# Kernel tuning notes

Measured on AMD Instinct MI355X. Metric: run time of the kernel, lower is better.

The kernel has to match this reference:

```python
import jax, jax.numpy as jnp
import numpy as np
import math

B, T, WIDTH, NUM_HEADS, WINDOW = 2, 2048, 1024, 16, 1024
HEAD_DIM = WIDTH // NUM_HEADS
_MIN_LOGITS_VALUE = -1e30


def setup_inputs() -> dict:
    key = jax.random.key(0)
    k1, k2, k3, k4, k5 = jax.random.split(key, 5)
    std = math.sqrt(1.0 / WIDTH)
    x = jax.random.normal(k1, (B, T, WIDTH), dtype=jnp.float32)
    segment_pos = jnp.tile(jnp.arange(T, dtype=jnp.int32)[None, :], (B, 1))
    Wq = jax.random.normal(k2, (WIDTH, WIDTH), dtype=jnp.float32) * std
    Wk = jax.random.normal(k3, (HEAD_DIM, WIDTH), dtype=jnp.float32) * std
    Wv = jax.random.normal(k4, (HEAD_DIM, WIDTH), dtype=jnp.float32) * std
    Wf = jax.random.normal(k5, (WIDTH, WIDTH), dtype=jnp.float32) * std
    bf = jnp.zeros((WIDTH,), dtype=jnp.float32)
    return {"x": x, "segment_pos": segment_pos, "Wq": Wq, "Wk": Wk, "Wv": Wv, "Wf": Wf, "bf": bf}


def reference(x, segment_pos, Wq, Wk, Wv, Wf, bf):
    b, t, _ = x.shape
    # projections (torch Linear: y = x @ W.T)
    q = (x @ Wq.T).reshape(b, t, NUM_HEADS, HEAD_DIM)  # b t n h
    k = x @ Wk.T  # b s h  (single shared KV head, MQA)
    v = x @ Wv.T  # b s h
    scale = 1.0 / math.sqrt(HEAD_DIM)
    logits = jnp.einsum('btnh,bsh->bnts', q, k) * scale
    pos = jnp.arange(t)
    q_pos = pos[:, None]
    k_pos = pos[None, :]
    mask = (q_pos >= k_pos) & (q_pos <= k_pos + WINDOW)  # [t, t]
    masked = jnp.where(mask[None, None, :, :], logits, _MIN_LOGITS_VALUE)
    probs = jax.nn.softmax(masked.astype(jnp.float32), axis=-1).astype(logits.dtype)
    out = jnp.einsum('bnts,bsh->btnh', probs, v).reshape(b, t, WIDTH)
    return out @ Wf.T + bf
```

## Files before the change

### kernel.cpp

```cpp
#include <hip/hip_runtime.h>
#include <cstdint>
#include <cstddef>

#define BB      2
#define TT      2048
#define WID     1024
#define NH      16
#define HD      64
#define WIN     1024
#define MROWS   (BB*TT)
#define NQKV    1152
#define QSCL    0.18033688011112042f

typedef __attribute__((ext_vector_type(8))) short  short8;
typedef __attribute__((ext_vector_type(4))) float  floatx4;

__device__ __forceinline__ unsigned short f2bf(float f) {
  union { float f; unsigned int u; } v; v.f = f;
  unsigned int u = v.u;
  unsigned int r = (u + 0x7fffu + ((u >> 16) & 1u)) >> 16;
  return (unsigned short)r;
}

__device__ __forceinline__ float fast_exp2(float x) {
#if __has_builtin(__builtin_amdgcn_exp2f)
  return __builtin_amdgcn_exp2f(x);
#else
  return exp2f(x);
#endif
}

__device__ __forceinline__ unsigned int pk_bf16_trunc(float lo, float hi) {
  union { float f; unsigned int u; } a, b; a.f = lo; b.f = hi;
#if __has_builtin(__builtin_amdgcn_perm)
  return __builtin_amdgcn_perm(b.u, a.u, 0x07060302u);
#else
  return (b.u & 0xffff0000u) | (a.u >> 16);
#endif
}

__device__ __forceinline__ void gld_lds16(const void* g, void* l) {
  __builtin_amdgcn_global_load_lds(
      (const __attribute__((address_space(1))) unsigned int*)g,
      (__attribute__((address_space(3))) unsigned int*)l, 16, 0, 0);
}

__global__ __launch_bounds__(256) void convert_kernel(
    const float* __restrict__ x,  const float* __restrict__ wq,
    const float* __restrict__ wk, const float* __restrict__ wv,
    const float* __restrict__ wf,
    unsigned short* __restrict__ xb, unsigned short* __restrict__ wb,
    unsigned short* __restrict__ wfb)
{
  const int NX4 = (MROWS * WID) / 4;
  const int NQ4 = (WID * WID) / 4;
  const int NK4 = (HD * WID) / 4;
  const int NW4 = NQ4 + 2 * NK4;
  const int NF4 = (WID * WID) / 4;
  const int TOT = NX4 + NW4 + NF4;
  for (int i = blockIdx.x * blockDim.x + threadIdx.x; i < TOT;
       i += gridDim.x * blockDim.x) {
    float4 v4;
    unsigned short* dptr;
    if (i < NX4) {
      v4 = ((const float4*)x)[i];
      dptr = xb + (size_t)i * 4;
    } else if (i < NX4 + NW4) {
      int k = i - NX4;
      dptr = wb + (size_t)k * 4;
      if (k < NQ4)            v4 = ((const float4*)wq)[k];
      else if (k < NQ4 + NK4) v4 = ((const float4*)wk)[k - NQ4];
      else                    v4 = ((const float4*)wv)[k - NQ4 - NK4];
    } else {
      int k = i - NX4 - NW4;
      v4 = ((const float4*)wf)[k];
      dptr = wfb + (size_t)k * 4;
    }
    ushort4 o4 = make_ushort4(f2bf(v4.x), f2bf(v4.y), f2bf(v4.z), f2bf(v4.w));
    *(ushort4*)dptr = o4;
  }
}

__global__ __launch_bounds__(256) void gemm128(
    const unsigned short* __restrict__ A, const unsigned short* __restrict__ Bm,
    int M, int N, int K, int mode,
    float* __restrict__ C, const float* __restrict__ bias,
    unsigned short* __restrict__ qb, unsigned short* __restrict__ kb,
    unsigned short* __restrict__ vtb)
{
  __shared__ __align__(16) unsigned short As[2][128 * 32];
  __shared__ __align__(16) unsigned short Bs[2][128 * 32];

  const int tid  = threadIdx.x;
  const int m0   = blockIdx.x * 128;
  const int n0   = blockIdx.y * 128;
  const int w    = tid >> 6;
  const int lane = tid & 63;
  const int wr   = w >> 1;
  const int wc   = w & 1;
  const int quad = lane >> 4;
  const int l16  = lane & 15;

  const int r0 = tid >> 2;
  const int c0 = (tid + r0) & 3;
  const unsigned short* gA0 = A  + (size_t)(m0 + r0) * K + c0 * 8;
  const unsigned short* gA1 = A  + (size_t)(m0 + r0 + 64) * K + c0 * 8;
  const unsigned short* gB0 = Bm + (size_t)(n0 + r0) * K + c0 * 8;
  const unsigned short* gB1 = Bm + (size_t)(n0 + r0 + 64) * K + c0 * 8;
  char* ldsA = (char*)As + (tid & 192) * 16;
  char* ldsB = (char*)Bs + (tid & 192) * 16;

  const int jsw = ((quad - l16) & 3) * 8;

  floatx4 acc[4][4];
#pragma unroll
  for (int it = 0; it < 4; ++it)
#pragma unroll
    for (int jt = 0; jt < 4; ++jt)
      acc[it][jt] = (floatx4){0.f, 0.f, 0.f, 0.f};

  const int K32 = K >> 5;
  gld_lds16(gA0, ldsA);
  gld_lds16(gA1, ldsA + 4096);
  gld_lds16(gB0, ldsB);
  gld_lds16(gB1, ldsB + 4096);
  __syncthreads();

  for (int kt = 0; kt < K32; ++kt) {
    const int cur = kt & 1;
    if (kt + 1 < K32) {
      const int nxt = cur ^ 1;
      const int off = (kt + 1) * 32;
      gld_lds16(gA0 + off, ldsA + nxt * 8192);
      gld_lds16(gA1 + off, ldsA + nxt * 8192 + 4096);
      gld_lds16(gB0 + off, ldsB + nxt * 8192);
      gld_lds16(gB1 + off, ldsB + nxt * 8192 + 4096);
    }
    const unsigned short* as = As[cur];
    const unsigned short* bs = Bs[cur];
    short8 af[4], bfr[4];
#pragma unroll
    for (int it = 0; it < 4; ++it)
      af[it] = *(const short8*)(as + (wr * 64 + it * 16 + l16) * 32 + jsw);
#pragma unroll
    for (int jt = 0; jt < 4; ++jt)
      bfr[jt] = *(const short8*)(bs + (wc * 64 + jt * 16 + l16) * 32 + jsw);

#pragma unroll
    for (int it = 0; it < 4; ++it)
#pragma unroll
      for (int jt = 0; jt < 4; ++jt)
        acc[it][jt] = __builtin_amdgcn_mfma_f32_16x16x32_bf16(
            af[it], bfr[jt], acc[it][jt], 0, 0, 0);
    __syncthreads();
  }

  if (mode == 0) {
#pragma unroll
    for (int it = 0; it < 4; ++it) {
      const int gr = m0 + wr * 64 + it * 16 + quad * 4;
#pragma unroll
      for (int jt = 0; jt < 4; ++jt) {
        const int gc = n0 + wc * 64 + jt * 16 + l16;
        const float badd = bias[gc];
#pragma unroll
        for (int r = 0; r < 4; ++r)
          C[(size_t)(gr + r) * N + gc] = acc[it][jt][r] + badd;
      }
    }
  } else {
#pragma unroll
    for (int it = 0; it < 4; ++it) {
      const int gr = m0 + wr * 64 + it * 16 + quad * 4;
#pragma unroll
      for (int jt = 0; jt < 4; ++jt) {
        const int gc = n0 + wc * 64 + jt * 16 + l16;
        if (gc < WID) {
#pragma unroll
          for (int r = 0; r < 4; ++r)
            qb[(size_t)(gr + r) * WID + gc] = f2bf(acc[it][jt][r] * QSCL);
        } else if (gc < WID + HD) {
#pragma unroll
          for (int r = 0; r < 4; ++r)
            kb[(size_t)(gr + r) * HD + (gc - WID)] = f2bf(acc[it][jt][r]);
        } else {
          ushort4 o4 = make_ushort4(f2bf(acc[it][jt][0]), f2bf(acc[it][jt][1]),
                                    f2bf(acc[it][jt][2]), f2bf(acc[it][jt][3]));
          *(ushort4*)(vtb + (size_t)(gc - WID - HD) * MROWS + gr) = o4;
        }
      }
    }
  }
}

__global__ __launch_bounds__(512) void attn_mfma(
    const unsigned short* __restrict__ qb, const unsigned short* __restrict__ kb,
    const unsigned short* __restrict__ vtb, unsigned short* __restrict__ attnb)
{
  __shared__ __align__(16) unsigned short smem[20480];

  const int tid  = threadIdx.x;
  const int w    = tid >> 6;
  const int g    = w >> 2;
  const int wh   = w & 3;
  const int lane = tid & 63;
  const int l16  = lane & 15;
  const int quad = lane >> 4;
  const int t0   = blockIdx.x * 32;
  const int h    = blockIdx.y * 4 + wh;
  const int b    = blockIdx.z;

  unsigned short* Ksb = smem;
  unsigned short* VTb = smem + 5120;
  unsigned short* Psb = smem + 10240 + w * 1280;

  short8 qf[2][2];
#pragma unroll
  for (int nt = 0; nt < 2; ++nt) {
    const unsigned short* qp =
        qb + (size_t)(b * TT + t0 + nt * 16 + l16) * WID + h * HD + quad * 8;
    qf[nt][0] = *(const short8*)qp;
    qf[nt][1] = *(const short8*)(qp + 32);
  }

  floatx4 Oacc[4][2];
#pragma unroll
  for (int mh = 0; mh < 4; ++mh)
#pragma unroll
    for (int nt = 0; nt < 2; ++nt)
      Oacc[mh][nt] = (floatx4){0.f, 0.f, 0.f, 0.f};
  float lq[2] = {0.f, 0.f};

  int s_begin = t0 - WIN; if (s_begin < 0) s_begin = 0;
  const int T = ((t0 + 32) - s_begin) >> 5;
  const int I = (T + 1) >> 1;

  const int kkey  = tid >> 3;
  const int khseg = (tid & 7) * 8;
  const int ksel  = kkey >> 5, krow = kkey & 31;
  const int vhd   = tid >> 3;
  const int vkk   = (tid & 7) * 8;
  const int vsel  = vkk >> 5,  vcol = vkk & 31;

  const unsigned short* kbase = kb  + (size_t)(b * TT) * HD;
  const unsigned short* vbase = vtb + (size_t)vhd * MROWS + b * TT;

  int s0p = s_begin;
  int ck = s0p + kkey; if (ck > TT - 1) ck = TT - 1;
  int cv = s0p + vkk;  if (cv > TT - 8) cv = TT - 8;
  short8 kreg = *(const short8*)(kbase + (size_t)ck * HD + khseg);
  short8 vreg = *(const short8*)(vbase + cv);

  for (int i = 0; i < I; ++i) {
    __syncthreads();
    *(short8*)(Ksb + ksel * 2560 + krow * 80 + khseg) = kreg;
    *(short8*)(VTb + vsel * 2560 + vhd * 40 + vcol)   = vreg;
    __syncthreads();
    if (i + 1 < I) {
      s0p += 64;
      ck = s0p + kkey; if (ck > TT - 1) ck = TT - 1;
      cv = s0p + vkk;  if (cv > TT - 8) cv = TT - 8;
      kreg = *(const short8*)(kbase + (size_t)ck * HD + khseg);
      vreg = *(const short8*)(vbase + cv);
    }

    const int ta = 2 * i + g;
    if (ta < T) {
      const int s0 = s_begin + ta * 32;
      const unsigned short* ks = Ksb + g * 2560;
      const unsigned short* vs = VTb + g * 2560;

      short8 kf[2][2];
#pragma unroll
      for (int mk = 0; mk < 2; ++mk)
#pragma unroll
        for (int k2 = 0; k2 < 2; ++k2)
          kf[mk][k2] = *(const short8*)(ks + (mk * 16 + l16) * 80 + k2 * 32 + quad * 8);

      floatx4 Sc[2][2];
#pragma unroll
      for (int mk = 0; mk < 2; ++mk)
#pragma unroll
        for (int nt = 0; nt < 2; ++nt)
          Sc[mk][nt] = (floatx4){0.f, 0.f, 0.f, 0.f};
#pragma unroll
      for (int mk = 0; mk < 2; ++mk)
#pragma unroll
        for (int nt = 0; nt < 2; ++nt)
#pragma unroll
          for (int k2 = 0; k2 < 2; ++k2)
            Sc[mk][nt] = __builtin_amdgcn_mfma_f32_16x16x32_bf16(
                kf[mk][k2], qf[nt][k2], Sc[mk][nt], 0, 0, 0);

      const int mode = (s0 == t0) ? 2 : ((t0 >= WIN && s0 == t0 - WIN) ? 1 : 0);

#pragma unroll
      for (int nt = 0; nt < 2; ++nt) {
        const int t = t0 + nt * 16 + l16;
        float p[8], ps = 0.f;
#pragma unroll
        for (int mk = 0; mk < 2; ++mk)
#pragma unroll
          for (int r = 0; r < 4; ++r) {
            float v = Sc[mk][nt][r];
            if (mode) {
              const int s = s0 + mk * 16 + quad * 4 + r;
              const bool kill = (mode == 2) ? (s > t) : (s + WIN < t);
              if (kill) v = -1.0e5f;
            }
            const float e = fast_exp2(v);
            p[mk * 4 + r] = e; ps += e;
          }
        ps += __shfl_xor(ps, 16);
        ps += __shfl_xor(ps, 32);
        lq[nt] += ps;
        uint2 w0 = make_uint2(pk_bf16_trunc(p[0], p[1]), pk_bf16_trunc(p[2], p[3]));
        uint2 w1 = make_uint2(pk_bf16_trunc(p[4], p[5]), pk_bf16_trunc(p[6], p[7]));
        *(uint2*)(Psb + (nt * 16 + l16) * 40 + quad * 4)      = w0;
        *(uint2*)(Psb + (nt * 16 + l16) * 40 + 16 + quad * 4) = w1;
      }

      short8 pf0 = *(const short8*)(Psb + l16 * 40 + quad * 8);
      short8 pf1 = *(const short8*)(Psb + (16 + l16) * 40 + quad * 8);
#pragma unroll
      for (int mh = 0; mh < 4; ++mh) {
        short8 vf = *(const short8*)(vs + (mh * 16 + l16) * 40 + quad * 8);
        Oacc[mh][0] = __builtin_amdgcn_mfma_f32_16x16x32_bf16(vf, pf0, Oacc[mh][0], 0, 0, 0);
        Oacc[mh][1] = __builtin_amdgcn_mfma_f32_16x16x32_bf16(vf, pf1, Oacc[mh][1], 0, 0, 0);
      }
    }
  }

  __syncthreads();
  float* mrg = (float*)smem;
  float* ob  = mrg + wh * 2336 + lane * 36;
  if (g == 1) {
#pragma unroll
    for (int mh = 0; mh < 4; ++mh)
#pragma unroll
      for (int nt = 0; nt < 2; ++nt)
        *(floatx4*)(ob + mh * 8 + nt * 4) = Oacc[mh][nt];
    if (quad == 0) {
      mrg[wh * 2336 + 2304 + l16]      = lq[0];
      mrg[wh * 2336 + 2304 + 16 + l16] = lq[1];
    }
  }
  __syncthreads();
  if (g == 0) {
    lq[0] += mrg[wh * 2336 + 2304 + l16];
    lq[1] += mrg[wh * 2336 + 2304 + 16 + l16];
#pragma unroll
    for (int nt = 0; nt < 2; ++nt) {
      const float inv = 1.f / lq[nt];
      unsigned short* op = attnb + (size_t)(b * TT + t0 + nt * 16 + l16) * WID
                         + h * HD + quad * 4;
#pragma unroll
      for (int mh = 0; mh < 4; ++mh) {
        floatx4 o1 = *(const floatx4*)(ob + mh * 8 + nt * 4);
        ushort4 o4 = make_ushort4(f2bf((Oacc[mh][nt][0] + o1[0]) * inv),
                                  f2bf((Oacc[mh][nt][1] + o1[1]) * inv),
                                  f2bf((Oacc[mh][nt][2] + o1[2]) * inv),
                                  f2bf((Oacc[mh][nt][3] + o1[3]) * inv));
        *(ushort4*)(op + mh * 16) = o4;
      }
    }
  }
}

extern "C" void kernel_launch(void* const* d_in, const int* in_sizes, int n_in,
                              void* d_out, int out_size, void* d_ws, size_t ws_size,
                              hipStream_t stream) {
  const float* x   = (const float*)d_in[0];
  const float* wq  = (const float*)d_in[2];
  const float* wk  = (const float*)d_in[3];
  const float* wv  = (const float*)d_in[4];
  const float* wf  = (const float*)d_in[5];
  const float* bfp = (const float*)d_in[6];
  float* out = (float*)d_out;

  char* ws = (char*)d_ws;
  unsigned short* xb   = (unsigned short*)(ws + 0);
  unsigned short* wb   = (unsigned short*)(ws + 8388608);
  unsigned short* wfb  = (unsigned short*)(ws + 10747904);
  unsigned short* qbuf = (unsigned short*)(ws + 12845056);
  unsigned short* kbuf = (unsigned short*)(ws + 21233664);
  unsigned short* vtb  = (unsigned short*)(ws + 21757952);
  unsigned short* attnb = xb;

  hipLaunchKernelGGL(convert_kernel, dim3(1024), dim3(256), 0, stream,
                     x, wq, wk, wv, wf, xb, wb, wfb);
  hipLaunchKernelGGL(gemm128, dim3(MROWS / 128, NQKV / 128), dim3(256), 0, stream,
                     xb, wb, MROWS, NQKV, WID, 1,
                     (float*)nullptr, (const float*)nullptr, qbuf, kbuf, vtb);
  hipLaunchKernelGGL(attn_mfma, dim3(TT / 32, NH / 4, BB), dim3(512), 0, stream,
                     qbuf, kbuf, vtb, attnb);
  hipLaunchKernelGGL(gemm128, dim3(MROWS / 128, WID / 128), dim3(256), 0, stream,
                     attnb, wfb, MROWS, WID, WID, 0,
                     out, bfp, (unsigned short*)nullptr, (unsigned short*)nullptr,
                     (unsigned short*)nullptr);
}
```

Measured before the change: 164.0 us.

## Retile GEMMs to 64x128 with K=64 steps and double-buffer attention K/V tiles

The projection GEMMs switch from 128x128 tiles with K-step 32 to 64x128 tiles with K-step 64. This doubles the grid to fill more of the GPU's compute units and halves the number of barrier iterations, using a new 8-way XOR swizzle for the LDS reads. The attention kernel double-buffers its K/V shared-memory tiles, which removes one __syncthreads per iteration, and moves the row-sum shuffle reduction out of the loop to run once at the end. In exchange, each GEMM tile reuses fewer A/B loads per MFMA, and the attention kernel uses more LDS, which may lower occupancy.

Result: faster. 150.8 us (-8.1%).

```diff
diff --git a/kernel.cpp b/kernel.cpp
--- a/kernel.cpp
+++ b/kernel.cpp
@@ -81,18 +81,18 @@
   }
 }
 
-__global__ __launch_bounds__(256) void gemm128(
+__global__ __launch_bounds__(256) void gemm64(
     const unsigned short* __restrict__ A, const unsigned short* __restrict__ Bm,
     int M, int N, int K, int mode,
     float* __restrict__ C, const float* __restrict__ bias,
     unsigned short* __restrict__ qb, unsigned short* __restrict__ kb,
     unsigned short* __restrict__ vtb)
 {
-  __shared__ __align__(16) unsigned short As[2][128 * 32];
-  __shared__ __align__(16) unsigned short Bs[2][128 * 32];
+  __shared__ __align__(16) unsigned short As[2][64 * 64];
+  __shared__ __align__(16) unsigned short Bs[2][128 * 64];
 
   const int tid  = threadIdx.x;
-  const int m0   = blockIdx.x * 128;
+  const int m0   = blockIdx.x * 64;
   const int n0   = blockIdx.y * 128;
   const int w    = tid >> 6;
   const int lane = tid & 63;
@@ -101,64 +101,77 @@
   const int quad = lane >> 4;
   const int l16  = lane & 15;
 
-  const int r0 = tid >> 2;
-  const int c0 = (tid + r0) & 3;
-  const unsigned short* gA0 = A  + (size_t)(m0 + r0) * K + c0 * 8;
-  const unsigned short* gA1 = A  + (size_t)(m0 + r0 + 64) * K + c0 * 8;
-  const unsigned short* gB0 = Bm + (size_t)(n0 + r0) * K + c0 * 8;
-  const unsigned short* gB1 = Bm + (size_t)(n0 + r0 + 64) * K + c0 * 8;
-  char* ldsA = (char*)As + (tid & 192) * 16;
-  char* ldsB = (char*)Bs + (tid & 192) * 16;
-
-  const int jsw = ((quad - l16) & 3) * 8;
-
-  floatx4 acc[4][4];
-#pragma unroll
-  for (int it = 0; it < 4; ++it)
+  const int rS  = tid >> 3;
+  const int cS  = tid & 7;
+  const int csS = (cS + rS) & 7;
+  const unsigned short* gA0 = A  + (size_t)(m0 + rS) * K + csS * 8;
+  const unsigned short* gA1 = gA0 + (size_t)32 * K;
+  const unsigned short* gB0 = Bm + (size_t)(n0 + rS) * K + csS * 8;
+  const unsigned short* gB1 = gB0 + (size_t)32 * K;
+  const unsigned short* gB2 = gB0 + (size_t)64 * K;
+  const unsigned short* gB3 = gB0 + (size_t)96 * K;
+  const int wub = (tid & 192) * 16;
+
+  floatx4 acc[2][4];
+#pragma unroll
+  for (int it = 0; it < 2; ++it)
 #pragma unroll
     for (int jt = 0; jt < 4; ++jt)
       acc[it][jt] = (floatx4){0.f, 0.f, 0.f, 0.f};
 
-  const int K32 = K >> 5;
-  gld_lds16(gA0, ldsA);
-  gld_lds16(gA1, ldsA + 4096);
-  gld_lds16(gB0, ldsB);
-  gld_lds16(gB1, ldsB + 4096);
+  const int K64 = K >> 6;
+  gld_lds16(gA0, (char*)As[0] + wub);
+  gld_lds16(gA1, (char*)As[0] + 4096 + wub);
+  gld_lds16(gB0, (char*)Bs[0] + wub);
+  gld_lds16(gB1, (char*)Bs[0] + 4096 + wub);
+  gld_lds16(gB2, (char*)Bs[0] + 8192 + wub);
+  gld_lds16(gB3, (char*)Bs[0] + 12288 + wub);
   __syncthreads();
 
-  for (int kt = 0; kt < K32; ++kt) {
+  for (int kt = 0; kt < K64; ++kt) {
     const int cur = kt & 1;
-    if (kt + 1 < K32) {
+    if (kt + 1 < K64) {
       const int nxt = cur ^ 1;
-      const int off = (kt + 1) * 32;
-      gld_lds16(gA0 + off, ldsA + nxt * 8192);
-      gld_lds16(gA1 + off, ldsA + nxt * 8192 + 4096);
-      gld_lds16(gB0 + off, ldsB + nxt * 8192);
-      gld_lds16(gB1 + off, ldsB + nxt * 8192 + 4096);
+      const int off = (kt + 1) * 64;
+      gld_lds16(gA0 + off, (char*)As[nxt] + wub);
+      gld_lds16(gA1 + off, (char*)As[nxt] + 4096 + wub);
+      gld_lds16(gB0 + off, (char*)Bs[nxt] + wub);
+      gld_lds16(gB1 + off, (char*)Bs[nxt] + 4096 + wub);
+      gld_lds16(gB2 + off, (char*)Bs[nxt] + 8192 + wub);
+      gld_lds16(gB3 + off, (char*)Bs[nxt] + 12288 + wub);
     }
     const unsigned short* as = As[cur];
     const unsigned short* bs = Bs[cur];
-    short8 af[4], bfr[4];
-#pragma unroll
-    for (int it = 0; it < 4; ++it)
-      af[it] = *(const short8*)(as + (wr * 64 + it * 16 + l16) * 32 + jsw);
-#pragma unroll
-    for (int jt = 0; jt < 4; ++jt)
-      bfr[jt] = *(const short8*)(bs + (wc * 64 + jt * 16 + l16) * 32 + jsw);
-
-#pragma unroll
-    for (int it = 0; it < 4; ++it)
-#pragma unroll
-      for (int jt = 0; jt < 4; ++jt)
-        acc[it][jt] = __builtin_amdgcn_mfma_f32_16x16x32_bf16(
-            af[it], bfr[jt], acc[it][jt], 0, 0, 0);
+    short8 af[2][2], bfr[4][2];
+#pragma unroll
+    for (int it = 0; it < 2; ++it) {
+      const int m = wr * 32 + it * 16 + l16;
+#pragma unroll
+      for (int ks = 0; ks < 2; ++ks)
+        af[it][ks] = *(const short8*)(as + m * 64 + (((ks * 4 + quad) - m) & 7) * 8);
+    }
+#pragma unroll
+    for (int jt = 0; jt < 4; ++jt) {
+      const int n = wc * 64 + jt * 16 + l16;
+#pragma unroll
+      for (int ks = 0; ks < 2; ++ks)
+        bfr[jt][ks] = *(const short8*)(bs + n * 64 + (((ks * 4 + quad) - n) & 7) * 8);
+    }
+#pragma unroll
+    for (int ks = 0; ks < 2; ++ks)
+#pragma unroll
+      for (int it = 0; it < 2; ++it)
+#pragma unroll
+        for (int jt = 0; jt < 4; ++jt)
+          acc[it][jt] = __builtin_amdgcn_mfma_f32_16x16x32_bf16(
+              af[it][ks], bfr[jt][ks], acc[it][jt], 0, 0, 0);
     __syncthreads();
   }
 
   if (mode == 0) {
 #pragma unroll
-    for (int it = 0; it < 4; ++it) {
-      const int gr = m0 + wr * 64 + it * 16 + quad * 4;
+    for (int it = 0; it < 2; ++it) {
+      const int gr = m0 + wr * 32 + it * 16 + quad * 4;
 #pragma unroll
       for (int jt = 0; jt < 4; ++jt) {
         const int gc = n0 + wc * 64 + jt * 16 + l16;
@@ -170,8 +183,8 @@
     }
   } else {
 #pragma unroll
-    for (int it = 0; it < 4; ++it) {
-      const int gr = m0 + wr * 64 + it * 16 + quad * 4;
+    for (int it = 0; it < 2; ++it) {
+      const int gr = m0 + wr * 32 + it * 16 + quad * 4;
 #pragma unroll
       for (int jt = 0; jt < 4; ++jt) {
         const int gc = n0 + wc * 64 + jt * 16 + l16;
@@ -197,7 +210,7 @@
     const unsigned short* __restrict__ qb, const unsigned short* __restrict__ kb,
     const unsigned short* __restrict__ vtb, unsigned short* __restrict__ attnb)
 {
-  __shared__ __align__(16) unsigned short smem[20480];
+  __shared__ __align__(16) unsigned short smem[30720];
 
   const int tid  = threadIdx.x;
   const int w    = tid >> 6;
@@ -210,9 +223,7 @@
   const int h    = blockIdx.y * 4 + wh;
   const int b    = blockIdx.z;
 
-  unsigned short* Ksb = smem;
-  unsigned short* VTb = smem + 5120;
-  unsigned short* Psb = smem + 10240 + w * 1280;
+  unsigned short* Psb = smem + 20480 + w * 1280;
 
   short8 qf[2][2];
 #pragma unroll
@@ -252,9 +263,9 @@
   short8 vreg = *(const short8*)(vbase + cv);
 
   for (int i = 0; i < I; ++i) {
-    __syncthreads();
-    *(short8*)(Ksb + ksel * 2560 + krow * 80 + khseg) = kreg;
-    *(short8*)(VTb + vsel * 2560 + vhd * 40 + vcol)   = vreg;
+    const int buf = i & 1;
+    *(short8*)(smem + buf * 5120 + ksel * 2560 + krow * 80 + khseg) = kreg;
+    *(short8*)(smem + 10240 + buf * 5120 + vsel * 2560 + vhd * 40 + vcol) = vreg;
     __syncthreads();
     if (i + 1 < I) {
       s0p += 64;
@@ -267,8 +278,8 @@
     const int ta = 2 * i + g;
     if (ta < T) {
       const int s0 = s_begin + ta * 32;
-      const unsigned short* ks = Ksb + g * 2560;
-      const unsigned short* vs = VTb + g * 2560;
+      const unsigned short* ks = smem + buf * 5120 + g * 2560;
+      const unsigned short* vs = smem + 10240 + buf * 5120 + g * 2560;
 
       short8 kf[2][2];
 #pragma unroll
@@ -311,8 +322,6 @@
             const float e = fast_exp2(v);
             p[mk * 4 + r] = e; ps += e;
           }
-        ps += __shfl_xor(ps, 16);
-        ps += __shfl_xor(ps, 32);
         lq[nt] += ps;
         uint2 w0 = make_uint2(pk_bf16_trunc(p[0], p[1]), pk_bf16_trunc(p[2], p[3]));
         uint2 w1 = make_uint2(pk_bf16_trunc(p[4], p[5]), pk_bf16_trunc(p[6], p[7]));
@@ -330,6 +339,9 @@
       }
     }
   }
+
+  lq[0] += __shfl_xor(lq[0], 16); lq[0] += __shfl_xor(lq[0], 32);
+  lq[1] += __shfl_xor(lq[1], 16); lq[1] += __shfl_xor(lq[1], 32);
 
   __syncthreads();
   float* mrg = (float*)smem;
@@ -389,12 +401,12 @@
 
   hipLaunchKernelGGL(convert_kernel, dim3(1024), dim3(256), 0, stream,
                      x, wq, wk, wv, wf, xb, wb, wfb);
-  hipLaunchKernelGGL(gemm128, dim3(MROWS / 128, NQKV / 128), dim3(256), 0, stream,
+  hipLaunchKernelGGL(gemm64, dim3(MROWS / 64, NQKV / 128), dim3(256), 0, stream,
                      xb, wb, MROWS, NQKV, WID, 1,
                      (float*)nullptr, (const float*)nullptr, qbuf, kbuf, vtb);
   hipLaunchKernelGGL(attn_mfma, dim3(TT / 32, NH / 4, BB), dim3(512), 0, stream,
                      qbuf, kbuf, vtb, attnb);
-  hipLaunchKernelGGL(gemm128, dim3(MROWS / 128, WID / 128), dim3(256), 0, stream,
+  hipLaunchKernelGGL(gemm64, dim3(MROWS / 64, WID / 128), dim3(256), 0, stream,
                      attnb, wfb, MROWS, WID, WID, 0,
                      out, bfp, (unsigned short*)nullptr, (unsigned short*)nullptr,
                      (unsigned short*)nullptr);
```
